# Optimization experiments

Measured on AMD Instinct MI355X. Metric: run time of the kernel, lower is better.

## Reference

```python
import jax, jax.numpy as jnp
import numpy as np

B, D, T, H, O = 64, 512, 512, 1024, 1

def setup_inputs() -> dict:
    key = jax.random.key(0)
    ks = jax.random.split(key, 7)
    s = 1.0 / np.sqrt(H)  # torch LSTMCell init scale
    return {
        "x": jax.random.normal(ks[0], (B, D, T), dtype=jnp.float32),
        "W_ih": jax.random.uniform(ks[1], (4 * H, D), jnp.float32, -s, s),
        "W_hh": jax.random.uniform(ks[2], (4 * H, H), jnp.float32, -s, s),
        "b_ih": jax.random.uniform(ks[3], (4 * H,), jnp.float32, -s, s),
        "b_hh": jax.random.uniform(ks[4], (4 * H,), jnp.float32, -s, s),
        "W_out": jax.random.uniform(ks[5], (O, H), jnp.float32, -s, s),
        "b_out": jax.random.uniform(ks[6], (O,), jnp.float32, -s, s),
    }

def reference(x, W_ih, W_hh, b_ih, b_hh, W_out, b_out):
    # x: (B, D, T) -> scan over time in (T, B, D) layout
    b, _, t = x.shape
    h = W_hh.shape[1]
    xs = jnp.transpose(x, (2, 0, 1))  # (T, B, D)
    # Precompute input projections for all timesteps (same math as per-step x @ W_ih.T)
    xg = jnp.einsum('tbd,gd->tbg', xs, W_ih) + b_ih  # (T, B, 4H)

    def step(carry, xg_t):
        h_t, c_t = carry
        gates = xg_t + h_t @ W_hh.T + b_hh          # (B, 4H)
        i, f, g, o = jnp.split(gates, 4, axis=-1)    # torch gate order: i, f, g, o
        c_t = jax.nn.sigmoid(f) * c_t + jax.nn.sigmoid(i) * jnp.tanh(g)
        h_t = jax.nn.sigmoid(o) * jnp.tanh(c_t)
        return (h_t, c_t), h_t

    init = (jnp.zeros((b, h), x.dtype), jnp.zeros((b, h), x.dtype))
    _, hs = jax.lax.scan(step, init, xg)             # hs: (T, B, H)
    out = hs @ W_out.T + b_out                       # (T, B, O)
    return jnp.transpose(out, (1, 2, 0))             # (B, O, T) == torch.stack(outputs, dim=2)
```

## Files before the change

### kernel.cpp

```cpp
#include <hip/hip_runtime.h>
#include <cstddef>

#define WS_XT_OFF   0ull
#define WS_WF_OFF   33554432ull
#define WS_PK_OFF   46137344ull

typedef _Float16 f16x8 __attribute__((ext_vector_type(8)));
typedef float    f32x4 __attribute__((ext_vector_type(4)));
typedef unsigned short u16;
typedef unsigned int   u32;
typedef unsigned long long u64;

__device__ __forceinline__ u16 f2h(float f) {
  _Float16 h = (_Float16)f;
  return __builtin_bit_cast(u16, h);
}
__device__ __forceinline__ float sigm(float x) {
  return __builtin_amdgcn_rcpf(1.0f + __expf(-x));
}
__device__ __forceinline__ float tanh_fast(float x) {
  return 1.0f - 2.0f * __builtin_amdgcn_rcpf(__expf(2.0f * x) + 1.0f);
}

__global__ __launch_bounds__(256) void k_init(uint4* pkt16) {
  int t = blockIdx.x * 256 + threadIdx.x;
  pkt16[t] = uint4{0u, 0u, 0u, 0u};
}

__global__ __launch_bounds__(256) void k_xpose(const float* __restrict__ x,
                                               u16* __restrict__ xT) {
  __shared__ float lds[64][65];
  const int d0 = blockIdx.x * 64, t0 = blockIdx.y * 64, b = blockIdx.z;
  const int tid = threadIdx.x;
  const int tt = tid & 63, dr = tid >> 6;
  const float* xp = x + ((size_t)b * 512 + d0) * 512 + t0 + tt;
#pragma unroll
  for (int i = 0; i < 16; ++i) {
    int dd = i * 4 + dr;
    lds[dd][tt] = xp[(size_t)dd * 512];
  }
  __syncthreads();
  const int dp = tid & 31, rr = tid >> 5;
#pragma unroll
  for (int i = 0; i < 8; ++i) {
    int tt2 = i * 8 + rr;
    u32 lo = f2h(lds[dp * 2][tt2]);
    u32 hi = f2h(lds[dp * 2 + 1][tt2]);
    *(u32*)(xT + ((size_t)(t0 + tt2) * 64 + b) * 512 + d0 + dp * 2) = lo | (hi << 16);
  }
}

__global__ __launch_bounds__(256) void k_wfrag(const float* __restrict__ W_ih,
                                               const float* __restrict__ W_hh,
                                               u16* __restrict__ Wf) {
  int g = blockIdx.x * 256 + threadIdx.x;
  int lane = g & 63;
  int c  = g >> 6;
  int mt = c & 3;
  int cc = c >> 2;
  int ks = cc % 48;
  int r  = cc / 48;
  int m = lane & 15, q = lane >> 4;
  int gate = m & 3;
  int j = r * 16 + mt * 4 + (m >> 2);
  int row = gate * 1024 + j;
  const float* src = (ks < 16) ? (W_ih + (size_t)row * 512 + ks * 32 + q * 8)
                               : (W_hh + (size_t)row * 1024 + (ks - 16) * 32 + q * 8);
  union { u16 s[8]; uint4 v; } U;
#pragma unroll
  for (int i = 0; i < 8; ++i) U.s[i] = f2h(src[i]);
  *(uint4*)(Wf + ((size_t)c * 64 + lane) * 8) = U.v;
}

__global__ __launch_bounds__(512, 2) void k_lstm(
    const u16* __restrict__ xT, const u16* __restrict__ Wf,
    u64* pkt,
    const float* __restrict__ b_ih, const float* __restrict__ b_hh,
    const float* __restrict__ W_out, float* __restrict__ part) {
  __shared__ f32x4 red[2][8 * 4 * 64];
  __shared__ u32 sh_as;
  const int tid = threadIdx.x;
  const int w = tid >> 6, lane = tid & 63;

  u32* cc = (u32*)(pkt + 32768);

  if (tid == 0) {
    u32 xcc;
    asm volatile("s_getreg_b32 %0, hwreg(HW_REG_XCC_ID)" : "=s"(xcc));
    xcc &= 7u;
    u32 sel = 0u, slot = 0u;
    for (int i = 0; i < 8; ++i) {
      u32 x = (xcc + (u32)i) & 7u;
      u32 s = __hip_atomic_fetch_add(cc + x * 32, 1u,
                                     __ATOMIC_RELAXED, __HIP_MEMORY_SCOPE_AGENT);
      if (s < 32u) { sel = x; slot = s; break; }
    }
    sh_as = (sel << 8) | slot;
  }
  __syncthreads();
  const u32 as = sh_as;
  const int g = (int)((as >> 8) >> 1);
  const int r = (int)(((as >> 8) & 1u) | ((as & 255u) << 1));
  const int bg0 = g * 16, j0 = r * 16;
  const int n = lane & 15, q = lane >> 4;

  f16x8 wfr[6][4];
#pragma unroll
  for (int kl = 0; kl < 6; ++kl) {
    int ks = (kl < 2) ? (2 * w + kl) : (16 + 4 * w + (kl - 2));
#pragma unroll
    for (int mt = 0; mt < 4; ++mt) {
      size_t c = ((size_t)r * 48 + ks) * 4 + mt;
      wfr[kl][mt] = *(const f16x8*)(Wf + (c * 64 + lane) * 8);
    }
  }

  float bias0 = 0.f, bias1 = 0.f, bias2 = 0.f, bias3 = 0.f, wout = 0.f;
  if (w < 4) {
    int j = j0 + w * 4 + q;
    bias0 = b_ih[j]        + b_hh[j];
    bias1 = b_ih[1024 + j] + b_hh[1024 + j];
    bias2 = b_ih[2048 + j] + b_hh[2048 + j];
    bias3 = b_ih[3072 + j] + b_hh[3072 + j];
    wout  = W_out[j];
  }

  size_t cb[4];
#pragma unroll
  for (int kl = 0; kl < 4; ++kl) {
    int p = (4 * w + kl) * 2 + (q >> 1);
    cb[kl] = ((((size_t)g * 64 + p) * 4 + (size_t)((q & 1) * 2)) * 16 + n) * 2;
  }
  const size_t pwb = ((((size_t)g * 64 + r) * 4 + w) * 16 + (lane & 15)) * 2;

  __syncthreads();
  if (tid == 0) {
    __hip_atomic_fetch_add(cc + 256, 1u, __ATOMIC_RELAXED, __HIP_MEMORY_SCOPE_AGENT);
    while (__hip_atomic_load(cc + 256, __ATOMIC_RELAXED, __HIP_MEMORY_SCOPE_AGENT) < 256u)
      __builtin_amdgcn_s_sleep(8);
  }
  __syncthreads();
  {
    f32x4 z = {0.f, 0.f, 0.f, 0.f};
    f32x4* p4 = (f32x4*)&part[((size_t)(tid * 4 + g) * 64 + r) * 16];
    p4[0] = z; p4[1] = z; p4[2] = z; p4[3] = z;
  }
  __syncthreads();
  asm volatile("" ::: "memory");

  float c_state = 0.f;
  const f32x4 zero = {0.f, 0.f, 0.f, 0.f};

  for (int t = 0; t < 512; ++t) {
    const u16* xtb = xT + (size_t)t * 32768;

    f16x8 bfr[6];
#pragma unroll
    for (int kl = 0; kl < 2; ++kl)
      bfr[kl] = *(const f16x8*)(xtb + (bg0 + n) * 512 + (2 * w + kl) * 32 + q * 8);

    f32x4 acc[4];
#pragma unroll
    for (int mt = 0; mt < 4; ++mt)
      acc[mt] = __builtin_amdgcn_mfma_f32_16x16x32_f16(wfr[0][mt], bfr[0], zero, 0, 0, 0);
#pragma unroll
    for (int mt = 0; mt < 4; ++mt)
      acc[mt] = __builtin_amdgcn_mfma_f32_16x16x32_f16(wfr[1][mt], bfr[1], acc[mt], 0, 0, 0);
#pragma unroll
    for (int mt = 0; mt < 4; ++mt) asm volatile("" : "+v"(acc[mt]));

    u64 a0[4], b0[4], a1[4], b1[4];
    {
      const u64* pb = pkt + (size_t)(t & 1) * 32768;
      const u32 et = (u32)t;
      for (;;) {
        bool ok = true;
#pragma unroll
        for (int kl = 0; kl < 4; ++kl) {
          const u64* p = pb + cb[kl];
          a0[kl] = __hip_atomic_load(p,      __ATOMIC_RELAXED, __HIP_MEMORY_SCOPE_AGENT);
          b0[kl] = __hip_atomic_load(p + 1,  __ATOMIC_RELAXED, __HIP_MEMORY_SCOPE_AGENT);
          a1[kl] = __hip_atomic_load(p + 32, __ATOMIC_RELAXED, __HIP_MEMORY_SCOPE_AGENT);
          b1[kl] = __hip_atomic_load(p + 33, __ATOMIC_RELAXED, __HIP_MEMORY_SCOPE_AGENT);
        }
#pragma unroll
        for (int kl = 0; kl < 4; ++kl) {
          ok = ok & ((u32)(a0[kl] >> 48) == et)
                  & (((u32)(b0[kl] >> 16) & 0xffffu) == et)
                  & ((u32)(a1[kl] >> 48) == et)
                  & (((u32)(b1[kl] >> 16) & 0xffffu) == et);
        }
        if (__all((int)ok)) break;
      }
    }
    asm volatile("" ::: "memory");

#pragma unroll
    for (int kl = 0; kl < 4; ++kl) {
      union { u32 u[4]; f16x8 v; } Bu;
      Bu.u[0] = (u32)a0[kl];
      Bu.u[1] = ((u32)(a0[kl] >> 32) & 0xffffu) | (((u32)b0[kl] & 0xffffu) << 16);
      Bu.u[2] = (u32)a1[kl];
      Bu.u[3] = ((u32)(a1[kl] >> 32) & 0xffffu) | (((u32)b1[kl] & 0xffffu) << 16);
      bfr[kl + 2] = Bu.v;
    }

#pragma unroll
    for (int kl = 2; kl < 6; ++kl)
#pragma unroll
      for (int mt = 0; mt < 4; ++mt)
        acc[mt] = __builtin_amdgcn_mfma_f32_16x16x32_f16(wfr[kl][mt], bfr[kl], acc[mt], 0, 0, 0);

#pragma unroll
    for (int mt = 0; mt < 4; ++mt)
      red[t & 1][(w * 4 + mt) * 64 + lane] = acc[mt];
    __syncthreads();

    if (w < 4) {
      const int mt = w;
      const f32x4* rp = &red[t & 1][mt * 64 + lane];
      f32x4 s01 = rp[0]    + rp[256];
      f32x4 s23 = rp[512]  + rp[768];
      f32x4 s45 = rp[1024] + rp[1280];
      f32x4 s67 = rp[1536] + rp[1792];
      f32x4 s = (s01 + s23) + (s45 + s67);
      float gi = s.x + bias0, gf = s.y + bias1, gg = s.z + bias2, go = s.w + bias3;
      c_state = sigm(gf) * c_state + sigm(gi) * tanh_fast(gg);
      float h = sigm(go) * tanh_fast(c_state);

      u32 hv  = (u32)__builtin_bit_cast(u16, (_Float16)h);
      u32 o16 = (u32)__shfl_xor((int)hv, 16);
      u32 pair = (hv & 0xffffu) | (o16 << 16);
      u32 o32 = (u32)__shfl_xor((int)pair, 32);
      if (lane < 16) {
        u64 tg = (u64)(u32)(t + 1);
        u64 Apkt = (u64)pair | ((u64)(o32 & 0xffffu) << 32) | (tg << 48);
        u64 Bpkt = (u64)((o32 >> 16) & 0xffffu) | (tg << 16);
        u64* pp = pkt + (size_t)((t + 1) & 1) * 32768 + pwb;
        __hip_atomic_store(pp,     Apkt, __ATOMIC_RELAXED, __HIP_MEMORY_SCOPE_AGENT);
        __hip_atomic_store(pp + 1, Bpkt, __ATOMIC_RELAXED, __HIP_MEMORY_SCOPE_AGENT);
      }
      float p = h * wout;
      p += __shfl_xor(p, 16);
      p += __shfl_xor(p, 32);
      if (lane < 16)
        __hip_atomic_fetch_add(&part[((size_t)(t * 4 + g) * 64 + r) * 16 + lane], p,
                               __ATOMIC_RELAXED, __HIP_MEMORY_SCOPE_WORKGROUP);
    }
  }
}

__global__ __launch_bounds__(256) void k_out(const float* __restrict__ part,
                                             const float* __restrict__ b_out,
                                             float* __restrict__ out) {
  int gi = blockIdx.x * 256 + threadIdx.x;
  int t = gi >> 6, b = gi & 63, g = b >> 4, b16 = b & 15;
  const float* p = part + ((size_t)(t * 4 + g) * 64) * 16 + b16;
  float s = b_out[0];
#pragma unroll 8
  for (int r = 0; r < 64; ++r) s += p[r * 16];
  out[(size_t)b * 512 + t] = s;
}

extern "C" void kernel_launch(void* const* d_in, const int* in_sizes, int n_in,
                              void* d_out, int out_size, void* d_ws, size_t ws_size,
                              hipStream_t stream) {
  const float* x    = (const float*)d_in[0];
  const float* W_ih = (const float*)d_in[1];
  const float* W_hh = (const float*)d_in[2];
  const float* b_ih = (const float*)d_in[3];
  const float* b_hh = (const float*)d_in[4];
  const float* Wout = (const float*)d_in[5];
  const float* bout = (const float*)d_in[6];
  float* out = (float*)d_out;

  unsigned char* ws = (unsigned char*)d_ws;
  u16* xT   = (u16*)(ws + WS_XT_OFF);
  u16* Wf   = (u16*)(ws + WS_WF_OFF);
  u64* pkt  = (u64*)(ws + WS_PK_OFF);
  float* part = (float*)(ws + WS_WF_OFF);

  k_init<<<512, 256, 0, stream>>>((uint4*)pkt);
  k_xpose<<<dim3(8, 8, 64), 256, 0, stream>>>(x, xT);
  k_wfrag<<<3072, 256, 0, stream>>>(W_ih, W_hh, Wf);

  void* args[7] = {&xT, &Wf, &pkt, &b_ih, &b_hh, &Wout, &part};
  hipLaunchCooperativeKernel((const void*)k_lstm, dim3(256), dim3(512), args, 0, stream);

  k_out<<<128, 256, 0, stream>>>(part, bout, out);
}
```

Before: 1.858 ms.

## Repartition LSTM grid to 8 batch groups by 32 hidden units per block

Changes the block decomposition from 4 batch groups of 16 with 16 hidden units per block to 8 batch groups of 8 with 32 hidden units per block. Each block now holds twice as many weight fragments in registers (8 M-tiles). All 8 waves now do the gate nonlinearities instead of 4, and launch bounds drop to one block per CU. The aim is to halve the hidden-state packets each block must poll and gather from peers each step, shrinking the synchronization fan-in. The cost is more register pressure and wasted MFMA columns, since only 8 of the 16 batch lanes carry real data.

Result: slower. 2.697 ms (+45.2%).

```diff
diff --git a/kernel.cpp b/kernel.cpp
--- a/kernel.cpp
+++ b/kernel.cpp
@@ -53,16 +53,16 @@
 __global__ __launch_bounds__(256) void k_wfrag(const float* __restrict__ W_ih,
                                                const float* __restrict__ W_hh,
                                                u16* __restrict__ Wf) {
-  int g = blockIdx.x * 256 + threadIdx.x;
-  int lane = g & 63;
-  int c  = g >> 6;
-  int mt = c & 3;
-  int cc = c >> 2;
+  int gidx = blockIdx.x * 256 + threadIdx.x;
+  int lane = gidx & 63;
+  int c  = gidx >> 6;
+  int mt = c & 7;
+  int cc = c >> 3;
   int ks = cc % 48;
   int r  = cc / 48;
   int m = lane & 15, q = lane >> 4;
   int gate = m & 3;
-  int j = r * 16 + mt * 4 + (m >> 2);
+  int j = r * 32 + mt * 4 + (m >> 2);
   int row = gate * 1024 + j;
   const float* src = (ks < 16) ? (W_ih + (size_t)row * 512 + ks * 32 + q * 8)
                                : (W_hh + (size_t)row * 1024 + (ks - 16) * 32 + q * 8);
@@ -72,12 +72,12 @@
   *(uint4*)(Wf + ((size_t)c * 64 + lane) * 8) = U.v;
 }
 
-__global__ __launch_bounds__(512, 2) void k_lstm(
+__global__ __launch_bounds__(512, 1) void k_lstm(
     const u16* __restrict__ xT, const u16* __restrict__ Wf,
     u64* pkt,
     const float* __restrict__ b_ih, const float* __restrict__ b_hh,
     const float* __restrict__ W_out, float* __restrict__ part) {
-  __shared__ f32x4 red[2][8 * 4 * 64];
+  __shared__ f32x4 red[2][8 * 8 * 64];
   __shared__ u32 sh_as;
   const int tid = threadIdx.x;
   const int w = tid >> 6, lane = tid & 63;
@@ -99,24 +99,25 @@
   }
   __syncthreads();
   const u32 as = sh_as;
-  const int g = (int)((as >> 8) >> 1);
-  const int r = (int)(((as >> 8) & 1u) | ((as & 255u) << 1));
-  const int bg0 = g * 16, j0 = r * 16;
+  const int g = (int)(as >> 8);
+  const int r = (int)(as & 255u);
+  const int bg0 = g * 8, j0 = r * 32;
   const int n = lane & 15, q = lane >> 4;
-
-  f16x8 wfr[6][4];
+  const int b8 = n & 7;
+
+  f16x8 wfr[6][8];
 #pragma unroll
   for (int kl = 0; kl < 6; ++kl) {
     int ks = (kl < 2) ? (2 * w + kl) : (16 + 4 * w + (kl - 2));
 #pragma unroll
-    for (int mt = 0; mt < 4; ++mt) {
-      size_t c = ((size_t)r * 48 + ks) * 4 + mt;
+    for (int mt = 0; mt < 8; ++mt) {
+      size_t c = ((size_t)r * 48 + ks) * 8 + mt;
       wfr[kl][mt] = *(const f16x8*)(Wf + (c * 64 + lane) * 8);
     }
   }
 
-  float bias0 = 0.f, bias1 = 0.f, bias2 = 0.f, bias3 = 0.f, wout = 0.f;
-  if (w < 4) {
+  float bias0, bias1, bias2, bias3, wout;
+  {
     int j = j0 + w * 4 + q;
     bias0 = b_ih[j]        + b_hh[j];
     bias1 = b_ih[1024 + j] + b_hh[1024 + j];
@@ -128,10 +129,10 @@
   size_t cb[4];
 #pragma unroll
   for (int kl = 0; kl < 4; ++kl) {
-    int p = (4 * w + kl) * 2 + (q >> 1);
-    cb[kl] = ((((size_t)g * 64 + p) * 4 + (size_t)((q & 1) * 2)) * 16 + n) * 2;
-  }
-  const size_t pwb = ((((size_t)g * 64 + r) * 4 + w) * 16 + (lane & 15)) * 2;
+    int rp = 4 * w + kl;
+    cb[kl] = ((((size_t)g * 32 + rp) * 8 + (size_t)(2 * q)) * 8 + b8) * 2;
+  }
+  const size_t pwb = ((((size_t)g * 32 + r) * 8 + w) * 8 + b8) * 2;
 
   __syncthreads();
   if (tid == 0) {
@@ -142,8 +143,8 @@
   __syncthreads();
   {
     f32x4 z = {0.f, 0.f, 0.f, 0.f};
-    f32x4* p4 = (f32x4*)&part[((size_t)(tid * 4 + g) * 64 + r) * 16];
-    p4[0] = z; p4[1] = z; p4[2] = z; p4[3] = z;
+    f32x4* p4 = (f32x4*)&part[(((size_t)tid * 8 + g) * 32 + r) * 8];
+    p4[0] = z; p4[1] = z;
   }
   __syncthreads();
   asm volatile("" ::: "memory");
@@ -157,17 +158,17 @@
     f16x8 bfr[6];
 #pragma unroll
     for (int kl = 0; kl < 2; ++kl)
-      bfr[kl] = *(const f16x8*)(xtb + (bg0 + n) * 512 + (2 * w + kl) * 32 + q * 8);
-
-    f32x4 acc[4];
-#pragma unroll
-    for (int mt = 0; mt < 4; ++mt)
+      bfr[kl] = *(const f16x8*)(xtb + (bg0 + b8) * 512 + (2 * w + kl) * 32 + q * 8);
+
+    f32x4 acc[8];
+#pragma unroll
+    for (int mt = 0; mt < 8; ++mt)
       acc[mt] = __builtin_amdgcn_mfma_f32_16x16x32_f16(wfr[0][mt], bfr[0], zero, 0, 0, 0);
 #pragma unroll
-    for (int mt = 0; mt < 4; ++mt)
+    for (int mt = 0; mt < 8; ++mt)
       acc[mt] = __builtin_amdgcn_mfma_f32_16x16x32_f16(wfr[1][mt], bfr[1], acc[mt], 0, 0, 0);
 #pragma unroll
-    for (int mt = 0; mt < 4; ++mt) asm volatile("" : "+v"(acc[mt]));
+    for (int mt = 0; mt < 8; ++mt) asm volatile("" : "+v"(acc[mt]));
 
     u64 a0[4], b0[4], a1[4], b1[4];
     {
@@ -180,8 +181,8 @@
           const u64* p = pb + cb[kl];
           a0[kl] = __hip_atomic_load(p,      __ATOMIC_RELAXED, __HIP_MEMORY_SCOPE_AGENT);
           b0[kl] = __hip_atomic_load(p + 1,  __ATOMIC_RELAXED, __HIP_MEMORY_SCOPE_AGENT);
-          a1[kl] = __hip_atomic_load(p + 32, __ATOMIC_RELAXED, __HIP_MEMORY_SCOPE_AGENT);
-          b1[kl] = __hip_atomic_load(p + 33, __ATOMIC_RELAXED, __HIP_MEMORY_SCOPE_AGENT);
+          a1[kl] = __hip_atomic_load(p + 16, __ATOMIC_RELAXED, __HIP_MEMORY_SCOPE_AGENT);
+          b1[kl] = __hip_atomic_load(p + 17, __ATOMIC_RELAXED, __HIP_MEMORY_SCOPE_AGENT);
         }
 #pragma unroll
         for (int kl = 0; kl < 4; ++kl) {
@@ -208,21 +209,20 @@
 #pragma unroll
     for (int kl = 2; kl < 6; ++kl)
 #pragma unroll
-      for (int mt = 0; mt < 4; ++mt)
+      for (int mt = 0; mt < 8; ++mt)
         acc[mt] = __builtin_amdgcn_mfma_f32_16x16x32_f16(wfr[kl][mt], bfr[kl], acc[mt], 0, 0, 0);
 
 #pragma unroll
-    for (int mt = 0; mt < 4; ++mt)
-      red[t & 1][(w * 4 + mt) * 64 + lane] = acc[mt];
+    for (int mt = 0; mt < 8; ++mt)
+      red[t & 1][(w * 8 + mt) * 64 + lane] = acc[mt];
     __syncthreads();
 
-    if (w < 4) {
-      const int mt = w;
-      const f32x4* rp = &red[t & 1][mt * 64 + lane];
-      f32x4 s01 = rp[0]    + rp[256];
-      f32x4 s23 = rp[512]  + rp[768];
-      f32x4 s45 = rp[1024] + rp[1280];
-      f32x4 s67 = rp[1536] + rp[1792];
+    {
+      const f32x4* rp2 = &red[t & 1][w * 64 + lane];
+      f32x4 s01 = rp2[0]    + rp2[512];
+      f32x4 s23 = rp2[1024] + rp2[1536];
+      f32x4 s45 = rp2[2048] + rp2[2560];
+      f32x4 s67 = rp2[3072] + rp2[3584];
       f32x4 s = (s01 + s23) + (s45 + s67);
       float gi = s.x + bias0, gf = s.y + bias1, gg = s.z + bias2, go = s.w + bias3;
       c_state = sigm(gf) * c_state + sigm(gi) * tanh_fast(gg);
@@ -232,7 +232,7 @@
       u32 o16 = (u32)__shfl_xor((int)hv, 16);
       u32 pair = (hv & 0xffffu) | (o16 << 16);
       u32 o32 = (u32)__shfl_xor((int)pair, 32);
-      if (lane < 16) {
+      if (lane < 8) {
         u64 tg = (u64)(u32)(t + 1);
         u64 Apkt = (u64)pair | ((u64)(o32 & 0xffffu) << 32) | (tg << 48);
         u64 Bpkt = (u64)((o32 >> 16) & 0xffffu) | (tg << 16);
@@ -243,8 +243,8 @@
       float p = h * wout;
       p += __shfl_xor(p, 16);
       p += __shfl_xor(p, 32);
-      if (lane < 16)
-        __hip_atomic_fetch_add(&part[((size_t)(t * 4 + g) * 64 + r) * 16 + lane], p,
+      if (lane < 8)
+        __hip_atomic_fetch_add(&part[(((size_t)t * 8 + g) * 32 + r) * 8 + lane], p,
                                __ATOMIC_RELAXED, __HIP_MEMORY_SCOPE_WORKGROUP);
     }
   }
@@ -254,11 +254,11 @@
                                              const float* __restrict__ b_out,
                                              float* __restrict__ out) {
   int gi = blockIdx.x * 256 + threadIdx.x;
-  int t = gi >> 6, b = gi & 63, g = b >> 4, b16 = b & 15;
-  const float* p = part + ((size_t)(t * 4 + g) * 64) * 16 + b16;
+  int t = gi >> 6, b = gi & 63, g = b >> 3, b8 = b & 7;
+  const float* p = part + (((size_t)t * 8 + g) * 32) * 8 + b8;
   float s = b_out[0];
 #pragma unroll 8
-  for (int r = 0; r < 64; ++r) s += p[r * 16];
+  for (int r = 0; r < 32; ++r) s += p[r * 8];
   out[(size_t)b * 512 + t] = s;
 }
 
@@ -280,7 +280,7 @@
   u64* pkt  = (u64*)(ws + WS_PK_OFF);
   float* part = (float*)(ws + WS_WF_OFF);
 
-  k_init<<<512, 256, 0, stream>>>((uint4*)pkt);
+  k_init<<<128, 256, 0, stream>>>((uint4*)pkt);
   k_xpose<<<dim3(8, 8, 64), 256, 0, stream>>>(x, xT);
   k_wfrag<<<3072, 256, 0, stream>>>(W_ih, W_hh, Wf);
 
```
